# Performance work log

Measured on AMD Instinct MI355X. Metric: run time of the kernel, lower is better.

The kernel has to match this reference:

```python
import jax, jax.numpy as jnp
import numpy as np
from jax import lax

L, B, F = 1024, 2, 1024
E = 2
H = E * F          # ssm_features = 2048
N = 16             # state_dim
R = F // N         # dt_rank = 64
K = 4              # conv kernel size
DT_MIN, DT_MAX = 0.001, 0.1


def setup_inputs() -> dict:
    key = jax.random.key(0)
    ks = jax.random.split(key, 6)
    def w(k, shape, fan_in):
        return jax.random.normal(k, shape, jnp.float32) / np.float32(np.sqrt(fan_in))
    x = jax.random.normal(ks[0], (L, B, F), jnp.float32)
    W_in = w(ks[1], (F, 2 * H), F)
    W_conv = w(ks[2], (K, H // E, H), K * (H // E))  # flax Conv kernel (K, in/groups, out), groups=E
    b_conv = jnp.zeros((H,), jnp.float32)
    A_log = jnp.log(jnp.broadcast_to(jnp.arange(1, N + 1, dtype=jnp.float32), (H, N)))
    D = jnp.ones((H,), jnp.float32)
    W_ssm = w(ks[3], (H, R + 2 * N), H)
    W_dt = w(ks[4], (R, H), R)
    b_dt = jnp.zeros((H,), jnp.float32)
    W_out = w(ks[5], (H, F), H)
    return dict(x=x, W_in=W_in, W_conv=W_conv, b_conv=b_conv, A_log=A_log, D=D,
                W_ssm=W_ssm, W_dt=W_dt, b_dt=b_dt, W_out=W_out)


def _selective_scan(u, dt, A, Bm, Cm, D):
    # u, dt: (L,B,H); A: (H,N); Bm, Cm: (L,B,N); D: (H,)
    dt = jnp.clip(dt, DT_MIN, DT_MAX)
    dA = jnp.exp(jnp.einsum('lbh,hn->lbhn', dt, A))          # (L,B,H,N)
    dBu = jnp.einsum('lbh,lbn->lbhn', dt * u, Bm)            # (L,B,H,N)
    def comb(s, c):
        return (c[0] * s[0], c[0] * s[1] + c[1])
    _, xs = lax.associative_scan(comb, (dA, dBu), axis=0)
    y = jnp.einsum('lbn,lbhn->lbh', Cm, xs)
    return y + u * D


def reference(x, W_in, W_conv, b_conv, A_log, D, W_ssm, W_dt, b_dt, W_out):
    # in_proj (no bias) then split into ssm branch and gate residual
    h = x @ W_in                                             # (L,B,2H)
    xs, res = jnp.split(h, 2, axis=-1)                       # each (L,B,H)
    # causal grouped conv over time: rearrange (L,B,H)->(B,L,H), NWC layout
    xc = jnp.transpose(xs, (1, 0, 2))
    xc = lax.conv_general_dilated(
        xc, W_conv, window_strides=(1,), padding=[(K - 1, 0)],
        dimension_numbers=('NWC', 'WIO', 'NWC'), feature_group_count=E) + b_conv
    xs = jnp.transpose(xc, (1, 0, 2))                        # (L,B,H)
    u = jax.nn.silu(xs)
    # SSM
    A = -jnp.exp(A_log)                                      # (H,N)
    proj = u @ W_ssm                                         # (L,B,N+N+R)
    Bm = proj[..., :N]
    Cm = proj[..., N:2 * N]
    dt = proj[..., 2 * N:]
    delta = jax.nn.softplus(dt @ W_dt + b_dt)                # (L,B,H)
    y = _selective_scan(u, delta, A, Bm, Cm, D)
    # gate and out_proj (no bias)
    return (y * jax.nn.silu(res)) @ W_out                    # (L,B,F)
```

## Files before the change

### kernel.cpp

```cpp
#include <hip/hip_runtime.h>
#include <math.h>


typedef unsigned short u16;
typedef unsigned int u32;
typedef __attribute__((ext_vector_type(8))) short short8;
typedef __attribute__((ext_vector_type(4))) float floatx4;
typedef __attribute__((ext_vector_type(4))) u16 ushort4v;

__device__ __forceinline__ u16 f2bf(float f) {
    u32 u = __float_as_uint(f);
    return (u16)((u + 0x7fffu + ((u >> 16) & 1u)) >> 16);
}
__device__ __forceinline__ float bf2f(u16 v) {
    return __uint_as_float((u32)v << 16);
}

__device__ __forceinline__ float dpp_red16(float v) {
    v += __uint_as_float((u32)__builtin_amdgcn_update_dpp(
        0, (int)__float_as_uint(v), 0xB1, 0xF, 0xF, true));
    v += __uint_as_float((u32)__builtin_amdgcn_update_dpp(
        0, (int)__float_as_uint(v), 0x4E, 0xF, 0xF, true));
    v += __uint_as_float((u32)__builtin_amdgcn_update_dpp(
        0, (int)__float_as_uint(v), 0x141, 0xF, 0xF, true));
    v += __uint_as_float((u32)__builtin_amdgcn_update_dpp(
        0, (int)__float_as_uint(v), 0x128, 0xF, 0xF, true));
    return v;
}

__device__ __forceinline__ void gl_lds16(const u16* g, u16* l) {
    auto gp = reinterpret_cast<const __attribute__((address_space(1))) u32*>(
        reinterpret_cast<uintptr_t>(g));
    auto lp = reinterpret_cast<__attribute__((address_space(3))) u32*>(
        reinterpret_cast<uintptr_t>(l));
    __builtin_amdgcn_global_load_lds(gp, lp, 16, 0, 0);
}

__device__ __forceinline__ void trans_dev(const float* __restrict__ S,
                                          u16* __restrict__ D, int R, int C,
                                          int bx, int by)
{
    __shared__ u16 t[64][65];
    int br = bx * 64;
    int bc = by * 64;
    int c = threadIdx.x & 63;
    int r0 = threadIdx.x >> 6;
#pragma unroll
    for (int i = 0; i < 16; ++i) {
        int r = r0 + i * 4;
        float v = 0.f;
        if (br + r < R && bc + c < C) v = S[(size_t)(br + r) * C + bc + c];
        t[r][c] = f2bf(v);
    }
    __syncthreads();
    int cc0 = threadIdx.x >> 4;
    int rr0 = (threadIdx.x & 15) * 4;
#pragma unroll
    for (int i = 0; i < 4; ++i) {
        int cc = i * 16 + cc0;
        if (bc + cc < C) {
            ushort4v o;
#pragma unroll
            for (int k = 0; k < 4; ++k) o[k] = t[rr0 + k][cc];
            *(ushort4v*)(D + (size_t)(bc + cc) * R + br + rr0) = o;
        }
    }
}

__global__ __launch_bounds__(256) void prep_k(
    const float* __restrict__ Wc, u16* __restrict__ WTc,
    const float* __restrict__ Wi, u16* __restrict__ WTi,
    const float* __restrict__ Wo, u16* __restrict__ WTo,
    const float* __restrict__ Ws, u16* __restrict__ WTs,
    const float* __restrict__ Wd, u16* __restrict__ WTd,
    const float* __restrict__ x,  u16* __restrict__ xb)
{
    int b = blockIdx.x;
    if (b < 2048) { trans_dev(Wc, WTc, 4096, 2048, b & 63, b >> 6); return; }
    b -= 2048;
    if (b < 1024) { trans_dev(Wi, WTi, 1024, 4096, b & 15, b >> 4); return; }
    b -= 1024;
    if (b < 512)  { trans_dev(Wo, WTo, 2048, 1024, b & 31, b >> 5); return; }
    b -= 512;
    if (b < 64)   { trans_dev(Ws, WTs, 2048, 96,   b & 31, b >> 5); return; }
    b -= 64;
    if (b < 32)   { trans_dev(Wd, WTd, 64, 2048,   0,      b);      return; }
    b -= 32;
    {
        int i = (b * 256 + threadIdx.x) * 4;
        float4 v = *(const float4*)(x + i);
        u16 o[4] = {f2bf(v.x), f2bf(v.y), f2bf(v.z), f2bf(v.w)};
        *(ulong1*)(xb + i) = *(ulong1*)o;
    }
}

__global__ __launch_bounds__(256) void tbf_k(const u16* __restrict__ S,
                                             u16* __restrict__ D)
{
    __shared__ u16 t[64][68];
    int br = blockIdx.x * 64;
    int bc = blockIdx.y * 64;
    int c = threadIdx.x & 63;
    int r0 = threadIdx.x >> 6;
#pragma unroll
    for (int i = 0; i < 16; ++i) {
        int r = r0 + i * 4;
        t[r][c] = S[(size_t)(br + r) * 2048 + bc + c];
    }
    __syncthreads();
#pragma unroll
    for (int i = 0; i < 16; ++i) {
        int r = r0 + i * 4;
        D[(size_t)(bc + r) * 2048 + br + c] = t[c][r];
    }
}

__global__ __launch_bounds__(256) void cvtp_k(const float* __restrict__ proj,
                                              u16* __restrict__ pb,
                                              u16* __restrict__ bc)
{
    if (blockIdx.x < 128) {
        int g = blockIdx.x * 256 + threadIdx.x;
        int m = g >> 4, i = (g & 15) * 4;
        float4 v = *(const float4*)(proj + (size_t)m * 128 + 64 + i);
        u16 o[4] = {f2bf(v.x), f2bf(v.y), f2bf(v.z), f2bf(v.w)};
        *(ulong1*)(pb + (size_t)m * 64 + i) = *(ulong1*)o;
    } else {
        int g = (blockIdx.x - 128) * 256 + threadIdx.x;
        int m = g >> 3, i = (g & 7) * 4;
        float4 v = *(const float4*)(proj + (size_t)m * 128 + i);
        u16 o[4] = {f2bf(v.x), f2bf(v.y), f2bf(v.z), f2bf(v.w)};
        *(ulong1*)(bc + (size_t)m * 32 + i) = *(ulong1*)o;
    }
}

template<int MODE>
__global__ __launch_bounds__(256) void gls_k(
    const u16* __restrict__ A, int lda,
    const u16* __restrict__ B, int ldb,
    float* __restrict__ Cf, int ldc,
    u16* __restrict__ Cb0, u16* __restrict__ Cb1,
    const float* __restrict__ bias, int nkt)
{
    __shared__ u16 As[128 * 64];
    __shared__ u16 Bs[64 * 64];
    const int tid = threadIdx.x;
    const int bm = blockIdx.y * 128;
    const int bn = blockIdx.x * 64;
    const int kofs = (MODE == 3) ? blockIdx.z * nkt * 64 : 0;
    const int gofs = (MODE == 1 && bn >= 1024) ? 1024 : 0;
    const int lane = tid & 63, wave = tid >> 6, wm = wave * 32;
    const int m16 = lane & 15, q = lane >> 4;
    floatx4 acc[2][4] = {};

    const int rsub = lane >> 3;
    const int pch  = lane & 7;

    for (int kt = 0; kt < nkt; ++kt) {
        const int k0 = kofs + kt * 64;
        int tap = 0, ck = k0;
        if (MODE == 1) { tap = k0 >> 10; ck = k0 & 1023; }
#pragma unroll
        for (int i = 0; i < 4; ++i) {
            int r = i * 32 + wave * 8 + rsub;
            int c = pch ^ (r & 7);
            const u16* g;
            if (MODE == 1) {
                int rg = bm + r + 2 * tap - 6;
                g = A + (size_t)rg * lda + gofs + ck + c * 8;
            } else {
                g = A + (size_t)(bm + r) * lda + k0 + c * 8;
            }
            gl_lds16(g, As + i * 2048 + wave * 512);
        }
#pragma unroll
        for (int i = 0; i < 2; ++i) {
            int r = i * 32 + wave * 8 + rsub;
            int c = pch ^ (r & 7);
            gl_lds16(B + (size_t)(bn + r) * ldb + k0 + c * 8,
                     Bs + i * 2048 + wave * 512);
        }
        if (MODE == 1 && bm == 0) {
            int zr = 6 - 2 * tap;
            if (zr > 0) {
                asm volatile("s_waitcnt vmcnt(0)" ::: "memory");
                if (tid < 64) {
                    int r = tid >> 3;
                    if (r < zr) *(short8*)(As + r * 64 + (tid & 7) * 8) = short8{};
                }
            }
        }
        __syncthreads();

#pragma unroll
        for (int ks = 0; ks < 2; ++ks) {
            short8 af[2], bfr[4];
#pragma unroll
            for (int ti = 0; ti < 2; ++ti) {
                int r = wm + ti * 16 + m16;
                int p = (ks * 4 + q) ^ (r & 7);
                af[ti] = *(const short8*)(As + r * 64 + p * 8);
            }
#pragma unroll
            for (int tj = 0; tj < 4; ++tj) {
                int r = tj * 16 + m16;
                int p = (ks * 4 + q) ^ (r & 7);
                bfr[tj] = *(const short8*)(Bs + r * 64 + p * 8);
            }
#pragma unroll
            for (int ti = 0; ti < 2; ++ti)
#pragma unroll
                for (int tj = 0; tj < 4; ++tj)
                    acc[ti][tj] = __builtin_amdgcn_mfma_f32_16x16x32_bf16(
                        af[ti], bfr[tj], acc[ti][tj], 0, 0, 0);
        }
        __syncthreads();
    }

    if (MODE == 3) {
#pragma unroll
        for (int tj = 0; tj < 4; ++tj) {
            int gn = bn + tj * 16 + m16;
#pragma unroll
            for (int ti = 0; ti < 2; ++ti) {
                int gm0 = bm + wm + ti * 16 + q * 4;
#pragma unroll
                for (int r = 0; r < 4; ++r)
                    atomicAdd(Cf + (size_t)(gm0 + r) * ldc + gn, acc[ti][tj][r]);
            }
        }
        return;
    }
    if (MODE == 0 && bn >= 2048) {
#pragma unroll
        for (int tj = 0; tj < 4; ++tj) {
            int gn = bn + tj * 16 + m16;
#pragma unroll
            for (int ti = 0; ti < 2; ++ti) {
                int gm0 = bm + wm + ti * 16 + q * 4;
                ushort4v h;
#pragma unroll
                for (int r = 0; r < 4; ++r) h[r] = f2bf(acc[ti][tj][r]);
                *(ushort4v*)(Cb1 + (size_t)(gn - 2048) * 2048 + gm0) = h;
            }
        }
        return;
    }
#pragma unroll
    for (int tj = 0; tj < 4; ++tj) {
        int gn = bn + tj * 16 + m16;
        float bv = (MODE == 1) ? bias[gn] : 0.f;
#pragma unroll
        for (int ti = 0; ti < 2; ++ti) {
            int lr0 = wm + ti * 16 + q * 4;
            ushort4v h;
#pragma unroll
            for (int r = 0; r < 4; ++r) {
                float v = acc[ti][tj][r];
                if (MODE == 1) {
                    v += bv;
                    v = v / (1.f + __expf(-v));
                }
                u16 hv = f2bf(v);
                h[r] = hv;
                As[(lr0 + r) * 64 + tj * 16 + m16] = hv;
            }
            if (MODE == 1)
                *(ushort4v*)(Cb1 + (size_t)gn * 2048 + bm + lr0) = h;
        }
    }
    __syncthreads();
    {
        int row = tid >> 1, half = tid & 1;
        u16* gdst = Cb0 + (size_t)(bm + row) * 2048 + bn + half * 32;
        const u16* lsrc = As + row * 64 + half * 32;
#pragma unroll
        for (int i = 0; i < 4; ++i)
            *(short8*)(gdst + i * 8) = *(const short8*)(lsrc + i * 8);
    }
}

#define APAD 40
__global__ __launch_bounds__(256) void g3_k(
    const u16* __restrict__ A,
    const u16* __restrict__ Bw,
    float* __restrict__ proj)
{
    __shared__ u16 As[128 * APAD];
    __shared__ u16 Bs[64 * APAD];
    const int tid = threadIdx.x;
    const int bn = blockIdx.x * 64;
    const int bm = blockIdx.y * 128;
    const int kb = blockIdx.z * 256;
    const int lane = tid & 63, wave = tid >> 6, wm = wave * 32;
    const int m16 = lane & 15, q = lane >> 4;
    floatx4 acc[2][4] = {};
    const int ar = tid >> 2, ac = (tid & 3) * 8;

    for (int kt = 0; kt < 8; ++kt) {
        const int k0 = kb + kt * 32;
#pragma unroll
        for (int p = 0; p < 2; ++p) {
            int r = ar + p * 64;
            *(short8*)(As + r * APAD + ac) =
                *(const short8*)(A + (size_t)(bm + r) * 2048 + k0 + ac);
        }
        *(short8*)(Bs + ar * APAD + ac) =
            *(const short8*)(Bw + (size_t)(bn + ar) * 2048 + k0 + ac);
        __syncthreads();

        short8 af[2], bfr[4];
#pragma unroll
        for (int ti = 0; ti < 2; ++ti)
            af[ti] = *(const short8*)(As + (wm + ti * 16 + m16) * APAD + q * 8);
#pragma unroll
        for (int tj = 0; tj < 4; ++tj)
            bfr[tj] = *(const short8*)(Bs + (tj * 16 + m16) * APAD + q * 8);
#pragma unroll
        for (int ti = 0; ti < 2; ++ti)
#pragma unroll
            for (int tj = 0; tj < 4; ++tj)
                acc[ti][tj] = __builtin_amdgcn_mfma_f32_16x16x32_bf16(
                    af[ti], bfr[tj], acc[ti][tj], 0, 0, 0);
        __syncthreads();
    }

#pragma unroll
    for (int tj = 0; tj < 4; ++tj) {
        int gn = bn + tj * 16 + m16;
        if (gn >= 96) continue;
        int col = (gn < 16) ? (2 * gn) : (gn < 32 ? 2 * (gn - 16) + 1 : 32 + gn);
#pragma unroll
        for (int ti = 0; ti < 2; ++ti)
#pragma unroll
            for (int r = 0; r < 4; ++r) {
                int gm = bm + wm + ti * 16 + q * 4 + r;
                atomicAdd(proj + (size_t)gm * 128 + col, acc[ti][tj][r]);
            }
    }
}

__global__ __launch_bounds__(256) void g4_k(
    const u16* __restrict__ A,
    const u16* __restrict__ B,
    const float* __restrict__ bias,
    float* __restrict__ Cf)
{
    __shared__ u16 As[128 * APAD];
    __shared__ u16 Bs[64 * APAD];
    const int tid = threadIdx.x;
    const int bm = blockIdx.y * 128;
    const int bn = blockIdx.x * 64;
    const int lane = tid & 63, wave = tid >> 6, wm = wave * 32;
    const int m16 = lane & 15, q = lane >> 4;
    floatx4 acc[2][4] = {};
    const int ar = tid >> 2, ac = (tid & 3) * 8;

    for (int kt = 0; kt < 2; ++kt) {
        const int k0 = kt * 32;
#pragma unroll
        for (int p = 0; p < 2; ++p) {
            int r = ar + p * 64;
            *(short8*)(As + r * APAD + ac) =
                *(const short8*)(A + (size_t)(bm + r) * 64 + k0 + ac);
        }
        *(short8*)(Bs + ar * APAD + ac) =
            *(const short8*)(B + (size_t)(bn + ar) * 64 + k0 + ac);
        __syncthreads();
        short8 af[2], bfr[4];
#pragma unroll
        for (int ti = 0; ti < 2; ++ti)
            af[ti] = *(const short8*)(As + (wm + ti * 16 + m16) * APAD + q * 8);
#pragma unroll
        for (int tj = 0; tj < 4; ++tj)
            bfr[tj] = *(const short8*)(Bs + (tj * 16 + m16) * APAD + q * 8);
#pragma unroll
        for (int ti = 0; ti < 2; ++ti)
#pragma unroll
            for (int tj = 0; tj < 4; ++tj)
                acc[ti][tj] = __builtin_amdgcn_mfma_f32_16x16x32_bf16(
                    af[ti], bfr[tj], acc[ti][tj], 0, 0, 0);
        __syncthreads();
    }
#pragma unroll
    for (int tj = 0; tj < 4; ++tj) {
        int gn = bn + tj * 16 + m16;
        float bv = bias[gn];
#pragma unroll
        for (int ti = 0; ti < 2; ++ti) {
            int gm0 = bm + wm + ti * 16 + q * 4;
            float t[4];
#pragma unroll
            for (int r = 0; r < 4; ++r) {
                float v = acc[ti][tj][r] + bv;
                v = (v > 15.f) ? v : log1pf(__expf(v));
                t[r] = fminf(fmaxf(v, 0.001f), 0.1f);
            }
            *(float4*)(Cf + (size_t)gn * 2048 + gm0) =
                make_float4(t[0], t[1], t[2], t[3]);
        }
    }
}

__global__ __launch_bounds__(512) void scan7_k(
    const float* __restrict__ deltaT,
    const u16* __restrict__ uT,
    const u16* __restrict__ bc16,
    const float* __restrict__ A_log,
    const float* __restrict__ Dvec,
    const u16* __restrict__ resT,
    u16* __restrict__ zT)
{
    __shared__ float lP[2][32][16], lS[2][32][16], lI[2][32][16];
    __shared__ float yrow[2048];
    const int h = blockIdx.x;
    const int tid = threadIdx.x;
    const int n = tid & 15;
    const int c = tid >> 4;
    const int l0 = c * 32;

    const float An2 = -__expf(A_log[h * 16 + n]) * 1.442695041f;
    const float* drow = deltaT + (size_t)h * 2048;
    const u16*   urow = uT     + (size_t)h * 2048;

    float s0 = 0.f, s1 = 0.f, T0 = 0.f, T1 = 0.f;
    for (int j = 0; j < 32; ++j) {
        int l = l0 + j;
        float2 dtv = *(const float2*)(drow + 2 * l);
        u32 uv = *(const u32*)(urow + 2 * l);
        float uu0 = __uint_as_float(uv << 16);
        float uu1 = __uint_as_float(uv & 0xffff0000u);
        u32 w0 = *(const u32*)(bc16 + (size_t)(2 * l) * 32 + 2 * n);
        u32 w1 = *(const u32*)(bc16 + (size_t)(2 * l + 1) * 32 + 2 * n);
        float e0 = exp2f(dtv.x * An2);
        float e1 = exp2f(dtv.y * An2);
        s0 = fmaf(e0, s0, dtv.x * uu0 * __uint_as_float(w0 << 16));
        s1 = fmaf(e1, s1, dtv.y * uu1 * __uint_as_float(w1 << 16));
        T0 += dtv.x;
        T1 += dtv.y;
    }
    lP[0][c][n] = exp2f(T0 * An2); lS[0][c][n] = s0;
    lP[1][c][n] = exp2f(T1 * An2); lS[1][c][n] = s1;
    __syncthreads();
    if (tid < 32) {
        int bb = tid >> 4, nn = tid & 15;
        float X = 0.f;
#pragma unroll
        for (int cc = 0; cc < 32; ++cc) {
            lI[bb][cc][nn] = X;
            X = fmaf(lP[bb][cc][nn], X, lS[bb][cc][nn]);
        }
    }
    __syncthreads();

    s0 = lI[0][c][n];
    s1 = lI[1][c][n];
    const float Dh = Dvec[h];
    for (int j = 0; j < 32; ++j) {
        int l = l0 + j;
        float2 dtv = *(const float2*)(drow + 2 * l);
        u32 uv = *(const u32*)(urow + 2 * l);
        float uu0 = __uint_as_float(uv << 16);
        float uu1 = __uint_as_float(uv & 0xffff0000u);
        u32 w0 = *(const u32*)(bc16 + (size_t)(2 * l) * 32 + 2 * n);
        u32 w1 = *(const u32*)(bc16 + (size_t)(2 * l + 1) * 32 + 2 * n);
        float e0 = exp2f(dtv.x * An2);
        float e1 = exp2f(dtv.y * An2);
        s0 = fmaf(e0, s0, dtv.x * uu0 * __uint_as_float(w0 << 16));
        s1 = fmaf(e1, s1, dtv.y * uu1 * __uint_as_float(w1 << 16));
        float v0 = dpp_red16(__uint_as_float(w0 & 0xffff0000u) * s0);
        float v1 = dpp_red16(__uint_as_float(w1 & 0xffff0000u) * s1);
        if (n == 0) {
            yrow[2 * l]     = v0 + uu0 * Dh;
            yrow[2 * l + 1] = v1 + uu1 * Dh;
        }
    }
    __syncthreads();
    {
        int t0 = tid * 4;
        ushort4v rv = *(const ushort4v*)(resT + (size_t)h * 2048 + t0);
        u16 o[4];
#pragma unroll
        for (int i = 0; i < 4; ++i) {
            float r = bf2f(rv[i]);
            float y = yrow[t0 + i];
            o[i] = f2bf(y * (r / (1.f + __expf(-r))));
        }
        *(ulong1*)(zT + (size_t)h * 2048 + t0) = *(ulong1*)o;
    }
}

extern "C" void kernel_launch(void* const* d_in, const int* in_sizes, int n_in,
                              void* d_out, int out_size, void* d_ws, size_t ws_size,
                              hipStream_t stream)
{
    const float* x      = (const float*)d_in[0];
    const float* W_in   = (const float*)d_in[1];
    const float* W_conv = (const float*)d_in[2];
    const float* b_conv = (const float*)d_in[3];
    const float* A_log  = (const float*)d_in[4];
    const float* Dv     = (const float*)d_in[5];
    const float* W_ssm  = (const float*)d_in[6];
    const float* W_dt   = (const float*)d_in[7];
    const float* b_dt   = (const float*)d_in[8];
    const float* W_out  = (const float*)d_in[9];
    float* out = (float*)d_out;

    char* wsc = (char*)d_ws;
    u16*   xb     = (u16*)wsc;
    float* projb  = (float*)wsc;
    u16*   pb_dt  = (u16*)(wsc + (2u << 20));
    u16*   bc16   = (u16*)(wsc + (3u << 20));
    u16*   WT_in  = (u16*)(wsc + (4u << 20));
    u16*   u_mh   = (u16*)(wsc + (4u << 20));
    u16*   z_mh   = (u16*)(wsc + (4u << 20));
    u16*   xsbf   = (u16*)(wsc + (12u << 20));
    u16*   zT     = xsbf;
    u16*   resT   = (u16*)(wsc + (20u << 20));
    u16*   WT_cv  = (u16*)(wsc + (28u << 20));
    float* deltaT = (float*)(wsc + (28u << 20));
    u16*   uT     = (u16*)(wsc + (44u << 20));
    u16*   WT_out = (u16*)(wsc + (52u << 20));
    u16*   WT_ssm = (u16*)(wsc + (56u << 20));
    u16*   WT_dt  = (u16*)(wsc + (56u << 20) + (512u << 10));

    dim3 blk(256);

    prep_k<<<dim3(5728), blk, 0, stream>>>(
        W_conv, WT_cv, W_in, WT_in, W_out, WT_out, W_ssm, WT_ssm, W_dt, WT_dt,
        x, xb);

    hipMemsetAsync(out, 0, 2048 * 1024 * sizeof(float), stream);

    gls_k<0><<<dim3(64, 16), blk, 0, stream>>>(
        xb, 1024, WT_in, 1024, nullptr, 0, xsbf, resT, nullptr, 16);

    hipMemsetAsync(projb, 0, 2048 * 128 * sizeof(float), stream);

    gls_k<1><<<dim3(32, 16), blk, 0, stream>>>(
        xsbf, 2048, WT_cv, 4096, nullptr, 0, u_mh, uT, b_conv, 64);

    g3_k<<<dim3(2, 16, 8), blk, 0, stream>>>(u_mh, WT_ssm, projb);

    cvtp_k<<<dim3(192), blk, 0, stream>>>(projb, pb_dt, bc16);

    g4_k<<<dim3(32, 16), blk, 0, stream>>>(pb_dt, WT_dt, b_dt, deltaT);

    scan7_k<<<dim3(2048), dim3(512), 0, stream>>>(
        deltaT, uT, bc16, A_log, Dv, resT, zT);

    tbf_k<<<dim3(32, 32), blk, 0, stream>>>(zT, z_mh);

    gls_k<3><<<dim3(16, 16, 2), blk, 0, stream>>>(
        z_mh, 2048, WT_out, 2048, out, 1024, nullptr, nullptr, nullptr, 16);
}
```

Before: 339.5 us.

## Add dedicated conv kernel reusing one input strip across all four taps

Replaces the MODE 1 path of the generic GEMM with a dedicated conv kernel. It loads a 136-row input strip once per 64-channel chunk and applies all four conv taps from shifted LDS rows, where the old path reloaded the A tile for each tap. This cuts global and LDS reload traffic for the A operand, at the cost of more LDS (strip plus four B tiles) and lower occupancy. Separately, the scan kernel's exp2f calls are replaced with the hardware exp2 builtin to drop range-handling overhead.

```diff
diff --git a/kernel.cpp b/kernel.cpp
--- a/kernel.cpp
+++ b/kernel.cpp
@@ -14,6 +14,9 @@
 }
 __device__ __forceinline__ float bf2f(u16 v) {
     return __uint_as_float((u32)v << 16);
+}
+__device__ __forceinline__ float fexp2(float x) {
+    return __builtin_amdgcn_exp2f(x);
 }
 
 __device__ __forceinline__ float dpp_red16(float v) {
@@ -148,7 +151,6 @@
     const int bm = blockIdx.y * 128;
     const int bn = blockIdx.x * 64;
     const int kofs = (MODE == 3) ? blockIdx.z * nkt * 64 : 0;
-    const int gofs = (MODE == 1 && bn >= 1024) ? 1024 : 0;
     const int lane = tid & 63, wave = tid >> 6, wm = wave * 32;
     const int m16 = lane & 15, q = lane >> 4;
     floatx4 acc[2][4] = {};
@@ -158,20 +160,12 @@
 
     for (int kt = 0; kt < nkt; ++kt) {
         const int k0 = kofs + kt * 64;
-        int tap = 0, ck = k0;
-        if (MODE == 1) { tap = k0 >> 10; ck = k0 & 1023; }
 #pragma unroll
         for (int i = 0; i < 4; ++i) {
             int r = i * 32 + wave * 8 + rsub;
             int c = pch ^ (r & 7);
-            const u16* g;
-            if (MODE == 1) {
-                int rg = bm + r + 2 * tap - 6;
-                g = A + (size_t)rg * lda + gofs + ck + c * 8;
-            } else {
-                g = A + (size_t)(bm + r) * lda + k0 + c * 8;
-            }
-            gl_lds16(g, As + i * 2048 + wave * 512);
+            gl_lds16(A + (size_t)(bm + r) * lda + k0 + c * 8,
+                     As + i * 2048 + wave * 512);
         }
 #pragma unroll
         for (int i = 0; i < 2; ++i) {
@@ -180,16 +174,6 @@
             gl_lds16(B + (size_t)(bn + r) * ldb + k0 + c * 8,
                      Bs + i * 2048 + wave * 512);
         }
-        if (MODE == 1 && bm == 0) {
-            int zr = 6 - 2 * tap;
-            if (zr > 0) {
-                asm volatile("s_waitcnt vmcnt(0)" ::: "memory");
-                if (tid < 64) {
-                    int r = tid >> 3;
-                    if (r < zr) *(short8*)(As + r * 64 + (tid & 7) * 8) = short8{};
-                }
-            }
-        }
         __syncthreads();
 
 #pragma unroll
@@ -248,25 +232,12 @@
     }
 #pragma unroll
     for (int tj = 0; tj < 4; ++tj) {
-        int gn = bn + tj * 16 + m16;
-        float bv = (MODE == 1) ? bias[gn] : 0.f;
 #pragma unroll
         for (int ti = 0; ti < 2; ++ti) {
             int lr0 = wm + ti * 16 + q * 4;
-            ushort4v h;
-#pragma unroll
-            for (int r = 0; r < 4; ++r) {
-                float v = acc[ti][tj][r];
-                if (MODE == 1) {
-                    v += bv;
-                    v = v / (1.f + __expf(-v));
-                }
-                u16 hv = f2bf(v);
-                h[r] = hv;
-                As[(lr0 + r) * 64 + tj * 16 + m16] = hv;
-            }
-            if (MODE == 1)
-                *(ushort4v*)(Cb1 + (size_t)gn * 2048 + bm + lr0) = h;
+#pragma unroll
+            for (int r = 0; r < 4; ++r)
+                As[(lr0 + r) * 64 + tj * 16 + m16] = f2bf(acc[ti][tj][r]);
         }
     }
     __syncthreads();
@@ -274,6 +245,118 @@
         int row = tid >> 1, half = tid & 1;
         u16* gdst = Cb0 + (size_t)(bm + row) * 2048 + bn + half * 32;
         const u16* lsrc = As + row * 64 + half * 32;
+#pragma unroll
+        for (int i = 0; i < 4; ++i)
+            *(short8*)(gdst + i * 8) = *(const short8*)(lsrc + i * 8);
+    }
+}
+
+__global__ __launch_bounds__(256) void conv2_k(
+    const u16* __restrict__ A,
+    const u16* __restrict__ B,
+    const float* __restrict__ bias,
+    u16* __restrict__ Cb0,
+    u16* __restrict__ Cb1)
+{
+    __shared__ u16 Astrip[136 * 64];
+    __shared__ u16 Bs[4 * 64 * 64];
+    const int tid = threadIdx.x;
+    const int bm = blockIdx.y * 128;
+    const int bn = blockIdx.x * 64;
+    const int gofs = (bn >= 1024) ? 1024 : 0;
+    const int lane = tid & 63, wave = tid >> 6, wm = wave * 32;
+    const int m16 = lane & 15, q = lane >> 4;
+    floatx4 acc[2][4] = {};
+    const int rsub = lane >> 3;
+    const int pch  = lane & 7;
+
+    for (int ch = 0; ch < 16; ++ch) {
+        const int ck = ch * 64;
+#pragma unroll
+        for (int i = 0; i < 4; ++i) {
+            int r = i * 32 + wave * 8 + rsub;
+            int c = pch ^ (r & 7);
+            int rg = bm + r - 6;
+            if (rg < 0) rg = 0;
+            gl_lds16(A + (size_t)rg * 2048 + gofs + ck + c * 8,
+                     Astrip + i * 2048 + wave * 512);
+        }
+        if (wave == 0) {
+            int r = 128 + rsub;
+            int c = pch ^ (r & 7);
+            int rg = bm + r - 6;
+            if (rg > 2047) rg = 2047;
+            gl_lds16(A + (size_t)rg * 2048 + gofs + ck + c * 8,
+                     Astrip + 4 * 2048);
+        }
+#pragma unroll
+        for (int t = 0; t < 4; ++t)
+#pragma unroll
+            for (int i = 0; i < 2; ++i) {
+                int r = i * 32 + wave * 8 + rsub;
+                int c = pch ^ (r & 7);
+                gl_lds16(B + (size_t)(bn + r) * 4096 + t * 1024 + ck + c * 8,
+                         Bs + t * 4096 + i * 2048 + wave * 512);
+            }
+        if (bm == 0) {
+            asm volatile("s_waitcnt vmcnt(0)" ::: "memory");
+            if (tid < 48)
+                *(short8*)(Astrip + (tid >> 3) * 64 + (tid & 7) * 8) = short8{};
+        }
+        __syncthreads();
+
+#pragma unroll
+        for (int t = 0; t < 4; ++t) {
+#pragma unroll
+            for (int ks = 0; ks < 2; ++ks) {
+                short8 af[2], bfr[4];
+#pragma unroll
+                for (int ti = 0; ti < 2; ++ti) {
+                    int sr = wm + ti * 16 + m16 + 2 * t;
+                    int p = (ks * 4 + q) ^ (sr & 7);
+                    af[ti] = *(const short8*)(Astrip + sr * 64 + p * 8);
+                }
+#pragma unroll
+                for (int tj = 0; tj < 4; ++tj) {
+                    int br = tj * 16 + m16;
+                    int p = (ks * 4 + q) ^ (br & 7);
+                    bfr[tj] = *(const short8*)(Bs + t * 4096 + br * 64 + p * 8);
+                }
+#pragma unroll
+                for (int ti = 0; ti < 2; ++ti)
+#pragma unroll
+                    for (int tj = 0; tj < 4; ++tj)
+                        acc[ti][tj] = __builtin_amdgcn_mfma_f32_16x16x32_bf16(
+                            af[ti], bfr[tj], acc[ti][tj], 0, 0, 0);
+            }
+        }
+        __syncthreads();
+    }
+
+#pragma unroll
+    for (int tj = 0; tj < 4; ++tj) {
+        int gn = bn + tj * 16 + m16;
+        float bv = bias[gn];
+#pragma unroll
+        for (int ti = 0; ti < 2; ++ti) {
+            int lr0 = wm + ti * 16 + q * 4;
+            ushort4v h;
+#pragma unroll
+            for (int r = 0; r < 4; ++r) {
+                float v = acc[ti][tj][r] + bv;
+                v = v / (1.f + __expf(-v));
+                u16 hv = f2bf(v);
+                h[r] = hv;
+                Astrip[(lr0 + r) * 64 + tj * 16 + m16] = hv;
+            }
+            *(ushort4v*)(Cb1 + (size_t)gn * 2048 + bm + lr0) = h;
+        }
+    }
+    __syncthreads();
+    {
+        int row = tid >> 1, half = tid & 1;
+        u16* gdst = Cb0 + (size_t)(bm + row) * 2048 + bn + half * 32;
+        const u16* lsrc = Astrip + row * 64 + half * 32;
 #pragma unroll
         for (int i = 0; i < 4; ++i)
             *(short8*)(gdst + i * 8) = *(const short8*)(lsrc + i * 8);
@@ -432,15 +515,15 @@
         float uu1 = __uint_as_float(uv & 0xffff0000u);
         u32 w0 = *(const u32*)(bc16 + (size_t)(2 * l) * 32 + 2 * n);
         u32 w1 = *(const u32*)(bc16 + (size_t)(2 * l + 1) * 32 + 2 * n);
-        float e0 = exp2f(dtv.x * An2);
-        float e1 = exp2f(dtv.y * An2);
+        float e0 = fexp2(dtv.x * An2);
+        float e1 = fexp2(dtv.y * An2);
         s0 = fmaf(e0, s0, dtv.x * uu0 * __uint_as_float(w0 << 16));
         s1 = fmaf(e1, s1, dtv.y * uu1 * __uint_as_float(w1 << 16));
         T0 += dtv.x;
         T1 += dtv.y;
     }
-    lP[0][c][n] = exp2f(T0 * An2); lS[0][c][n] = s0;
-    lP[1][c][n] = exp2f(T1 * An2); lS[1][c][n] = s1;
+    lP[0][c][n] = fexp2(T0 * An2); lS[0][c][n] = s0;
+    lP[1][c][n] = fexp2(T1 * An2); lS[1][c][n] = s1;
     __syncthreads();
     if (tid < 32) {
         int bb = tid >> 4, nn = tid & 15;
@@ -464,8 +547,8 @@
         float uu1 = __uint_as_float(uv & 0xffff0000u);
         u32 w0 = *(const u32*)(bc16 + (size_t)(2 * l) * 32 + 2 * n);
         u32 w1 = *(const u32*)(bc16 + (size_t)(2 * l + 1) * 32 + 2 * n);
-        float e0 = exp2f(dtv.x * An2);
-        float e1 = exp2f(dtv.y * An2);
+        float e0 = fexp2(dtv.x * An2);
+        float e1 = fexp2(dtv.y * An2);
         s0 = fmaf(e0, s0, dtv.x * uu0 * __uint_as_float(w0 << 16));
         s1 = fmaf(e1, s1, dtv.y * uu1 * __uint_as_float(w1 << 16));
         float v0 = dpp_red16(__uint_as_float(w0 & 0xffff0000u) * s0);
@@ -537,8 +620,7 @@
 
     hipMemsetAsync(projb, 0, 2048 * 128 * sizeof(float), stream);
 
-    gls_k<1><<<dim3(32, 16), blk, 0, stream>>>(
-        xsbf, 2048, WT_cv, 4096, nullptr, 0, u_mh, uT, b_conv, 64);
+    conv2_k<<<dim3(32, 16), blk, 0, stream>>>(xsbf, WT_cv, b_conv, u_mh, uT);
 
     g3_k<<<dim3(2, 16, 8), blk, 0, stream>>>(u_mh, WT_ssm, projb);
 
```

New measurement: 317.8 us. 6.4% less time.
